# Optimization experiments

Measured on AMD Instinct MI355X. Metric: run time of the kernel, lower is better.

## Reference

```python
import jax, jax.numpy as jnp
import numpy as np
from jax import lax

PADDING = 1  # from init_kwargs; must equal (k-1)//2 so the residual add is shape-valid


def _conv_single(x, w):
    # x: [C_in, H, W], w: [C_out, C_in, kH, kW] -> [C_out, H, W]
    y = lax.conv_general_dilated(
        x[None],  # [1, C_in, H, W]
        w,
        window_strides=(1, 1),
        padding=[(PADDING, PADDING), (PADDING, PADDING)],
        dimension_numbers=("NCHW", "OIHW", "NCHW"),
    )
    return y[0]


def setup_inputs() -> dict:
    key = jax.random.key(0)
    k1, k2 = jax.random.split(key)
    B, C, H, W, K = 16, 128, 64, 64, 3
    inp = jax.random.normal(k1, (B, C, H, W), dtype=jnp.float32)
    # per-sample dynamic weights, scaled so conv output is O(1)
    weight = jax.random.normal(k2, (B, C, C, K, K), dtype=jnp.float32) * (1.0 / np.sqrt(C * K * K))
    return {"input": inp, "weight": weight}


def reference(input, weight):
    # per-sample conv2d with a different kernel per batch element + residual add
    residual = jax.vmap(_conv_single)(input, weight)  # [B, C, H, W]
    return input + residual
```

## Files before the change

kernel.cpp:

```cpp
#include <hip/hip_runtime.h>
#include <hip/hip_bf16.h>


typedef _Float16 h8 __attribute__((ext_vector_type(8)));
typedef _Float16 h2 __attribute__((ext_vector_type(2)));
typedef float f32x16 __attribute__((ext_vector_type(16)));
typedef float f4 __attribute__((ext_vector_type(4)));

#define MFMA32 __builtin_amdgcn_mfma_f32_32x32x16_f16

__global__ __launch_bounds__(256) void w_prepass(const float* __restrict__ W,
                                                 _Float16* __restrict__ wp) {
    __shared__ float raw[8 * 1153];
    const int bid = blockIdx.x;
    const int b   = bid >> 4;
    const int co0 = (bid & 15) * 8;
    const int t   = threadIdx.x;

    const float* src = W + (size_t)(b * 128 + co0) * 1152;
#pragma unroll
    for (int i = 0; i < 9; ++i) {
        int idx  = (i * 256 + t) * 4;
        f4 v     = *(const f4*)(src + idx);
        int co_l = idx / 1152;
        int rem  = idx - co_l * 1152;
        *(f4*)&raw[co_l * 1153 + rem] = v;
    }
    __syncthreads();

#pragma unroll
    for (int i = 0; i < 9; ++i) {
        int c    = i * 256 + t;
        int jh   = c & 1;
        int co_l = (c >> 1) & 7;
        int oct  = (c >> 4) & 3;
        int r    = c >> 6;
        int kw   = r % 3;
        int r2   = r / 3;
        int kc   = r2 & 3;
        int kh   = r2 >> 2;
        int cib  = kc * 32 + oct * 8 + jh * 4;
        _Float16 v0 = (_Float16)raw[co_l * 1153 + (cib + 0) * 9 + kh * 3 + kw];
        _Float16 v1 = (_Float16)raw[co_l * 1153 + (cib + 1) * 9 + kh * 3 + kw];
        _Float16 v2 = (_Float16)raw[co_l * 1153 + (cib + 2) * 9 + kh * 3 + kw];
        _Float16 v3 = (_Float16)raw[co_l * 1153 + (cib + 3) * 9 + kh * 3 + kw];
        size_t o = ((size_t)(b * 3 + kh) * 4 + kc) * 12288 +
                   (size_t)(kw * 4 + oct) * 1024 + (size_t)(co0 + co_l) * 8 + jh * 4;
        wp[o + 0] = v0; wp[o + 1] = v1; wp[o + 2] = v2; wp[o + 3] = v3;
    }
}


__global__ __launch_bounds__(256, 4) void conv_main(const float* __restrict__ X,
                                                    const _Float16* __restrict__ wp,
                                                    float* __restrict__ out) {
    __shared__ _Float16 sX[2 * 2112];

    const int t    = threadIdx.x;
    const int lane = t & 63;
    const int l31  = lane & 31;
    const int lhi  = lane >> 5;
    const int wv   = t >> 6;

    const int bid   = blockIdx.x;
    const int swz   = (bid & 7) * 128 + (bid >> 3);
    const int batch = swz >> 6;
    const int h     = swz & 63;

    const int p  = t >> 4;
    const int xq = (t & 15) * 4;

    f32x16 acc[2];
#pragma unroll
    for (int nt = 0; nt < 2; ++nt)
#pragma unroll
        for (int r = 0; r < 16; ++r) acc[nt][r] = 0.f;

    if (t < 16) {
        int pb = t >> 3, oct = (t >> 1) & 3, side = t & 1;
        h8 z = {};
        *(h8*)&sX[pb * 2112 + (oct * 66 + side * 65) * 8] = z;
    }

    f4 xa, xb;

    const int wrow = (lhi * 128 + wv * 32 + l31) * 8;

    auto load_x = [&](int s) {
        const int kh = s >> 2, kc = s & 3;
        const int yy = h + kh - 1;
        if (yy >= 0 && yy < 64) {
            const float* xp = X + ((size_t)(batch * 128 + kc * 32 + 2 * p) * 64 + yy) * 64 + xq;
            xa = *(const f4*)xp;
            xb = *(const f4*)(xp + 4096);
        } else {
            xa = (f4){0.f, 0.f, 0.f, 0.f};
            xb = (f4){0.f, 0.f, 0.f, 0.f};
        }
    };

    auto write_x = [&](int pb) {
        const int oct = p >> 2;
        const int sub = (p & 3) * 2;
#pragma unroll
        for (int k = 0; k < 4; ++k) {
            h2 v = {(_Float16)xa[k], (_Float16)xb[k]};
            *(h2*)&sX[pb * 2112 + (oct * 66 + xq + 1 + k) * 8 + sub] = v;
        }
    };

    auto compute = [&](int s, int pb) {
        const int kh = s >> 2, kc = s & 3;
        const _Float16* wbase = wp + ((size_t)(batch * 3 + kh) * 4 + kc) * 12288 + wrow;
        const _Float16* sXp = sX + pb * 2112;
#pragma unroll
        for (int ks = 0; ks < 6; ++ks) {
            const int kw = ks >> 1, kk = ks & 1;
            h8 af, bf[2];
            af = *(const h8*)&wbase[(size_t)((kw * 4 + kk * 2) * 128) * 8];
#pragma unroll
            for (int nt = 0; nt < 2; ++nt)
                bf[nt] = *(const h8*)&sXp[((kk * 2 + lhi) * 66 + nt * 32 + l31 + kw) * 8];
            __builtin_amdgcn_s_setprio(1);
#pragma unroll
            for (int nt = 0; nt < 2; ++nt)
                acc[nt] = MFMA32(af, bf[nt], acc[nt], 0, 0, 0);
            __builtin_amdgcn_s_setprio(0);
        }
    };

    load_x(0);
    write_x(0);
    __syncthreads();

    int pbuf = 0;
#pragma unroll 1
    for (int s = 0; s < 11; ++s) {
        load_x(s + 1);
        compute(s, pbuf);
        write_x(pbuf ^ 1);
        __syncthreads();
        pbuf ^= 1;
    }
    compute(11, pbuf);

#pragma unroll
    for (int nt = 0; nt < 2; ++nt)
#pragma unroll
        for (int rg = 0; rg < 16; ++rg) {
            int co = wv * 32 + (rg & 3) + 8 * (rg >> 2) + 4 * lhi;
            int x  = nt * 32 + l31;
            size_t o = ((size_t)(batch * 128 + co) * 64 + h) * 64 + x;
            out[o] = X[o] + acc[nt][rg];
        }
}

extern "C" void kernel_launch(void* const* d_in, const int* in_sizes, int n_in,
                              void* d_out, int out_size, void* d_ws, size_t ws_size,
                              hipStream_t stream) {
    const float* inp = (const float*)d_in[0];
    const float* wgt = (const float*)d_in[1];
    float* out = (float*)d_out;
    _Float16* wpk = (_Float16*)d_ws;

    w_prepass<<<256, 256, 0, stream>>>(wgt, wpk);
    conv_main<<<1024, 256, 0, stream>>>(inp, wpk, out);
}
```

Before: 117.7 us.

## Stage all three input rows in LDS upfront and drop per-stage double buffering

The conv kernel now loads all three input rows for every channel into shared memory in one prologue, packing 8 channels per h8 store, then runs the kh×kc MFMA loops with no further barriers. This replaces the 12-stage double-buffered load/compute pipeline and its 11 __syncthreads, cutting sync overhead and making LDS writes wider. In exchange, LDS use rises to about 50 KB per block, so launch bounds drop from 4 to 3 blocks per CU. Global-load latency is no longer overlapped with MFMA work inside a block.

```diff
diff --git a/kernel.cpp b/kernel.cpp
--- a/kernel.cpp
+++ b/kernel.cpp
@@ -3,7 +3,6 @@
 
 
 typedef _Float16 h8 __attribute__((ext_vector_type(8)));
-typedef _Float16 h2 __attribute__((ext_vector_type(2)));
 typedef float f32x16 __attribute__((ext_vector_type(16)));
 typedef float f4 __attribute__((ext_vector_type(4)));
 
@@ -51,10 +50,10 @@
 }
 
 
-__global__ __launch_bounds__(256, 4) void conv_main(const float* __restrict__ X,
+__global__ __launch_bounds__(256, 3) void conv_main(const float* __restrict__ X,
                                                     const _Float16* __restrict__ wp,
                                                     float* __restrict__ out) {
-    __shared__ _Float16 sX[2 * 2112];
+    __shared__ _Float16 sX[3 * 16 * 66 * 8];
 
     const int t    = threadIdx.x;
     const int lane = t & 63;
@@ -67,82 +66,66 @@
     const int batch = swz >> 6;
     const int h     = swz & 63;
 
-    const int p  = t >> 4;
-    const int xq = (t & 15) * 4;
-
     f32x16 acc[2];
 #pragma unroll
     for (int nt = 0; nt < 2; ++nt)
 #pragma unroll
         for (int r = 0; r < 16; ++r) acc[nt][r] = 0.f;
 
-    if (t < 16) {
-        int pb = t >> 3, oct = (t >> 1) & 3, side = t & 1;
+    if (t < 96) {
+        int y = t >> 5, oct = (t >> 1) & 15, side = t & 1;
         h8 z = {};
-        *(h8*)&sX[pb * 2112 + (oct * 66 + side * 65) * 8] = z;
+        *(h8*)&sX[((y * 16 + oct) * 66 + side * 65) * 8] = z;
     }
 
-    f4 xa, xb;
+    {
+        const int o  = t >> 4;
+        const int xq = (t & 15) * 4;
+#pragma unroll
+        for (int y = 0; y < 3; ++y) {
+            const int yy = h + y - 1;
+            f4 xr[8];
+            if (yy >= 0 && yy < 64) {
+                const float* xp = X + ((size_t)(batch * 128 + o * 8) * 64 + yy) * 64 + xq;
+#pragma unroll
+                for (int j = 0; j < 8; ++j) xr[j] = *(const f4*)(xp + (size_t)j * 4096);
+            } else {
+#pragma unroll
+                for (int j = 0; j < 8; ++j) xr[j] = (f4){0.f, 0.f, 0.f, 0.f};
+            }
+#pragma unroll
+            for (int k = 0; k < 4; ++k) {
+                h8 v = {(_Float16)xr[0][k], (_Float16)xr[1][k],
+                        (_Float16)xr[2][k], (_Float16)xr[3][k],
+                        (_Float16)xr[4][k], (_Float16)xr[5][k],
+                        (_Float16)xr[6][k], (_Float16)xr[7][k]};
+                *(h8*)&sX[((y * 16 + o) * 66 + xq + 1 + k) * 8] = v;
+            }
+        }
+    }
+    __syncthreads();
 
     const int wrow = (lhi * 128 + wv * 32 + l31) * 8;
-
-    auto load_x = [&](int s) {
-        const int kh = s >> 2, kc = s & 3;
-        const int yy = h + kh - 1;
-        if (yy >= 0 && yy < 64) {
-            const float* xp = X + ((size_t)(batch * 128 + kc * 32 + 2 * p) * 64 + yy) * 64 + xq;
-            xa = *(const f4*)xp;
-            xb = *(const f4*)(xp + 4096);
-        } else {
-            xa = (f4){0.f, 0.f, 0.f, 0.f};
-            xb = (f4){0.f, 0.f, 0.f, 0.f};
+#pragma unroll 1
+    for (int kh = 0; kh < 3; ++kh) {
+#pragma unroll 1
+        for (int kc = 0; kc < 4; ++kc) {
+            const _Float16* wbase = wp + ((size_t)(batch * 3 + kh) * 4 + kc) * 12288 + wrow;
+            const _Float16* xbase = sX + (size_t)(kh * 16 + kc * 4) * 528;
+#pragma unroll
+            for (int ks = 0; ks < 6; ++ks) {
+                const int kw = ks >> 1, kk = ks & 1;
+                h8 af, bf0, bf1;
+                af  = *(const h8*)&wbase[(size_t)((kw * 4 + kk * 2) * 128) * 8];
+                bf0 = *(const h8*)&xbase[((kk * 2 + lhi) * 66 + l31 + kw) * 8];
+                bf1 = *(const h8*)&xbase[((kk * 2 + lhi) * 66 + 32 + l31 + kw) * 8];
+                __builtin_amdgcn_s_setprio(1);
+                acc[0] = MFMA32(af, bf0, acc[0], 0, 0, 0);
+                acc[1] = MFMA32(af, bf1, acc[1], 0, 0, 0);
+                __builtin_amdgcn_s_setprio(0);
+            }
         }
-    };
-
-    auto write_x = [&](int pb) {
-        const int oct = p >> 2;
-        const int sub = (p & 3) * 2;
-#pragma unroll
-        for (int k = 0; k < 4; ++k) {
-            h2 v = {(_Float16)xa[k], (_Float16)xb[k]};
-            *(h2*)&sX[pb * 2112 + (oct * 66 + xq + 1 + k) * 8 + sub] = v;
-        }
-    };
-
-    auto compute = [&](int s, int pb) {
-        const int kh = s >> 2, kc = s & 3;
-        const _Float16* wbase = wp + ((size_t)(batch * 3 + kh) * 4 + kc) * 12288 + wrow;
-        const _Float16* sXp = sX + pb * 2112;
-#pragma unroll
-        for (int ks = 0; ks < 6; ++ks) {
-            const int kw = ks >> 1, kk = ks & 1;
-            h8 af, bf[2];
-            af = *(const h8*)&wbase[(size_t)((kw * 4 + kk * 2) * 128) * 8];
-#pragma unroll
-            for (int nt = 0; nt < 2; ++nt)
-                bf[nt] = *(const h8*)&sXp[((kk * 2 + lhi) * 66 + nt * 32 + l31 + kw) * 8];
-            __builtin_amdgcn_s_setprio(1);
-#pragma unroll
-            for (int nt = 0; nt < 2; ++nt)
-                acc[nt] = MFMA32(af, bf[nt], acc[nt], 0, 0, 0);
-            __builtin_amdgcn_s_setprio(0);
-        }
-    };
-
-    load_x(0);
-    write_x(0);
-    __syncthreads();
-
-    int pbuf = 0;
-#pragma unroll 1
-    for (int s = 0; s < 11; ++s) {
-        load_x(s + 1);
-        compute(s, pbuf);
-        write_x(pbuf ^ 1);
-        __syncthreads();
-        pbuf ^= 1;
     }
-    compute(11, pbuf);
 
 #pragma unroll
     for (int nt = 0; nt < 2; ++nt)
```

Result: slower. 134.8 us (+14.5%).
